# Kernel tuning notes

Measured on AMD Instinct MI355X. Metric: run time of the kernel, lower is better.

## Reference

```python
import jax, jax.numpy as jnp
import numpy as np

B, H, W = 4, 64, 64
DIM, NH, HD = 768, 12, 64
MLP_DIM = 3072
WS = 14
EPS = 1e-6
SCALE = HD ** -0.5
QMIN, QMAX = -128.0, 127.0  # 8-bit signed fake-quant range


def fake_quant(x, s):
    # uniform quant-dequant with straight-through estimator
    q = jnp.clip(jnp.round(x / s), QMIN, QMAX) * s
    return x + jax.lax.stop_gradient(q - x)


def layer_norm(x, w, b):
    mu = jnp.mean(x, axis=-1, keepdims=True)
    var = jnp.var(x, axis=-1, keepdims=True)
    return (x - mu) * jax.lax.rsqrt(var + EPS) * w + b


def qlinear(x, w, b, a_s, w_s):
    # PreQuantizedLayer: fake-quant input activation and weight, then linear
    return fake_quant(x, a_s) @ fake_quant(w, w_s).T + b


def _attention(xw, qkv_w, qkv_b, proj_w, proj_b, rel_pos_h, rel_pos_w, a_s, w_s):
    Bw = xw.shape[0]
    N = WS * WS
    qkv = qlinear(xw.reshape(Bw, N, DIM), qkv_w, qkv_b, a_s[4], w_s[0])
    qkv = qkv.reshape(Bw, N, 3, NH, HD).transpose(2, 0, 3, 1, 4).reshape(3, Bw * NH, N, HD)
    q = fake_quant(qkv[0], a_s[0])
    k = fake_quant(qkv[1], a_s[1])
    v = fake_quant(qkv[2], a_s[2])
    attn = jnp.einsum('bqc,bkc->bqk', q * SCALE, k)  # (Bw*NH, N, N)
    # decomposed relative position bias (q_size == k_size == WS)
    idx = jnp.arange(WS)[:, None] - jnp.arange(WS)[None, :] + (WS - 1)
    Rh = rel_pos_h[idx]  # (WS, WS, HD)
    Rw = rel_pos_w[idx]
    r_q = q.reshape(Bw * NH, WS, WS, HD)
    rel_h = jnp.einsum('bhwc,hkc->bhwk', r_q, Rh)
    rel_w = jnp.einsum('bhwc,wkc->bhwk', r_q, Rw)
    attn = (attn.reshape(-1, WS, WS, WS, WS) + rel_h[..., :, None] + rel_w[..., None, :]).reshape(-1, N, N)
    attn = fake_quant(jax.nn.softmax(attn, axis=-1), a_s[3])
    out = jnp.einsum('bqk,bkc->bqc', attn, v)
    out = out.reshape(Bw, NH, WS, WS, HD).transpose(0, 2, 3, 1, 4).reshape(Bw, WS, WS, DIM)
    return qlinear(out, proj_w, proj_b, a_s[5], w_s[1])


def _forward(x, ln1_w, ln1_b, ln2_w, ln2_b, qkv_w, qkv_b, proj_w, proj_b,
             lin1_w, lin1_b, lin2_w, lin2_b, rel_pos_h, rel_pos_w, act_scales, w_scales):
    shortcut = x
    h = layer_norm(x, ln1_w, ln1_b)
    pad_h = (WS - H % WS) % WS
    pad_w = (WS - W % WS) % WS
    Hp, Wp = H + pad_h, W + pad_w
    hp = jnp.pad(h, ((0, 0), (0, pad_h), (0, pad_w), (0, 0)))
    win = hp.reshape(B, Hp // WS, WS, Wp // WS, WS, DIM).transpose(0, 1, 3, 2, 4, 5).reshape(-1, WS, WS, DIM)
    win = _attention(win, qkv_w, qkv_b, proj_w, proj_b, rel_pos_h, rel_pos_w, act_scales, w_scales)
    hp = win.reshape(B, Hp // WS, Wp // WS, WS, WS, DIM).transpose(0, 1, 3, 2, 4, 5).reshape(B, Hp, Wp, DIM)
    x = shortcut + hp[:, :H, :W, :]
    y = layer_norm(x, ln2_w, ln2_b)
    y = qlinear(y, lin1_w, lin1_b, act_scales[6], w_scales[2])
    y = jax.nn.gelu(y, approximate=False)
    y = qlinear(y, lin2_w, lin2_b, act_scales[7], w_scales[3])
    return x + y


def setup_inputs() -> dict:
    key = jax.random.key(0)
    ks = jax.random.split(key, 12)
    def w(k, shape, std=0.02):
        return jax.random.normal(k, shape, dtype=jnp.float32) * std
    return {
        'x': jax.random.normal(ks[0], (B, H, W, DIM), dtype=jnp.float32),
        'ln1_w': jnp.ones((DIM,), jnp.float32), 'ln1_b': jnp.zeros((DIM,), jnp.float32),
        'ln2_w': jnp.ones((DIM,), jnp.float32), 'ln2_b': jnp.zeros((DIM,), jnp.float32),
        'qkv_w': w(ks[1], (3 * DIM, DIM)), 'qkv_b': jnp.zeros((3 * DIM,), jnp.float32),
        'proj_w': w(ks[2], (DIM, DIM)), 'proj_b': jnp.zeros((DIM,), jnp.float32),
        'lin1_w': w(ks[3], (MLP_DIM, DIM)), 'lin1_b': jnp.zeros((MLP_DIM,), jnp.float32),
        'lin2_w': w(ks[4], (DIM, MLP_DIM)), 'lin2_b': jnp.zeros((DIM,), jnp.float32),
        'rel_pos_h': w(ks[5], (2 * WS - 1, HD)), 'rel_pos_w': w(ks[6], (2 * WS - 1, HD)),
        'act_scales': jax.random.uniform(ks[7], (8,), jnp.float32, 0.01, 0.06),
        'w_scales': jax.random.uniform(ks[8], (4,), jnp.float32, 0.0005, 0.003),
    }


def reference(x, ln1_w, ln1_b, ln2_w, ln2_b, qkv_w, qkv_b, proj_w, proj_b,
              lin1_w, lin1_b, lin2_w, lin2_b, rel_pos_h, rel_pos_w, act_scales, w_scales):
    return _forward(x, ln1_w, ln1_b, ln2_w, ln2_b, qkv_w, qkv_b, proj_w, proj_b,
                    lin1_w, lin1_b, lin2_w, lin2_b, rel_pos_h, rel_pos_w, act_scales, w_scales)
```

## Files before the change

### kernel.cpp

```cpp
#include <hip/hip_runtime.h>
#include <cstdint>


typedef int   v4i __attribute__((ext_vector_type(4)));
typedef float v4f __attribute__((ext_vector_type(4)));
typedef short v8s __attribute__((ext_vector_type(8)));
typedef int8_t i8;

__device__ __forceinline__ i8 satq(float x) {
  float q = rintf(x);
  q = fminf(127.f, fmaxf(-128.f, q));
  return (i8)(int)q;
}

__device__ __forceinline__ void gload16(const i8* g, i8* l) {
  __builtin_amdgcn_global_load_lds((const __attribute__((address_space(1))) void*)g,
                                   (__attribute__((address_space(3))) void*)l, 16, 0, 0);
}

__device__ __forceinline__ int pack4(const i8* q) {
  return ((int)(unsigned char)q[0]) | ((int)(unsigned char)q[1] << 8) |
         ((int)(unsigned char)q[2] << 16) | ((int)(unsigned char)q[3] << 24);
}

__device__ __forceinline__ float fast_gelu(float v) {
  float x = fabsf(v) * 0.70710678118654752f;
  float t = __builtin_amdgcn_rcpf(fmaf(0.3275911f, x, 1.0f));
  float s = fmaf(1.061405429f, t, -1.453152027f);
  s = fmaf(s, t, 1.421413741f);
  s = fmaf(s, t, -0.284496736f);
  s = fmaf(s, t, 0.254829592f);
  s = s * t;
  float e = __expf(-x * x);
  float erfa = fmaf(-s, e, 1.0f);
  float erfs = copysignf(erfa, v);
  float hv = 0.5f * v;
  return fmaf(hv, erfs, hv);
}

__global__ __launch_bounds__(256) void k_wquant(const float* __restrict__ w,
                                                i8* __restrict__ o, int n16,
                                                const float* __restrict__ wsc, int sidx) {
  int i = blockIdx.x * 256 + threadIdx.x;
  if (i >= n16) return;
  float inv = 1.0f / wsc[sidx];
  const float4* src = (const float4*)w + (size_t)i * 4;
  i8 buf[16];
#pragma unroll
  for (int t = 0; t < 4; t++) {
    float4 f = src[t];
    buf[t*4+0] = satq(f.x * inv); buf[t*4+1] = satq(f.y * inv);
    buf[t*4+2] = satq(f.z * inv); buf[t*4+3] = satq(f.w * inv);
  }
  *(v4i*)(o + (size_t)i * 16) = *(v4i*)buf;
}

__global__ __launch_bounds__(256) void k_relpack(const float* __restrict__ rph,
    const float* __restrict__ rpw, short* __restrict__ TB) {
  int g = blockIdx.x * 256 + threadIdx.x;
  if (g >= 1024) return;
  int lane = g & 63, c = g >> 6;
  int p = c & 1, ks = (c >> 1) & 1, nt = (c >> 2) & 1, tb = c >> 3;
  const float* src = tb ? rpw : rph;
  int n = nt * 16 + (lane & 15);
  int k0 = ks * 32 + (lane >> 4) * 8;
  short outv[8];
#pragma unroll
  for (int j = 0; j < 8; j++) {
    float v = (n < 27) ? src[n * 64 + k0 + j] : 0.f;
    unsigned u = __float_as_uint(v);
    unsigned hi = (u + 0x7fffu + ((u >> 16) & 1u)) >> 16;
    if (p == 0) outv[j] = (short)hi;
    else {
      float lof = v - __uint_as_float(hi << 16);
      unsigned ul = __float_as_uint(lof);
      outv[j] = (short)((ul + 0x7fffu + ((ul >> 16) & 1u)) >> 16);
    }
  }
  *(v8s*)(TB + (size_t)c * 512 + lane * 8) = *(v8s*)outv;
}

__global__ __launch_bounds__(256) void k_ln1(const float* __restrict__ x,
    const float* __restrict__ w, const float* __restrict__ b,
    const float* __restrict__ as, i8* __restrict__ outq) {
  int wt = blockIdx.x * 4 + (threadIdx.x >> 6);
  int lane = threadIdx.x & 63;
  int win = wt / 196, tok = wt - win * 196;
  int bb = win / 25, wrem = win - bb * 25, wh = wrem / 5, ww = wrem - wh * 5;
  int r = tok / 14, c = tok - r * 14;
  int y = wh * 14 + r, xx = ww * 14 + c;
  i8* dst = outq + (size_t)wt * 768 + lane * 12;
  if (y >= 64 || xx >= 64) {
    ((int*)dst)[0] = 0; ((int*)dst)[1] = 0; ((int*)dst)[2] = 0;
    return;
  }
  const float* row = x + (((size_t)bb * 64 + y) * 64 + xx) * 768 + lane * 12;
  float v[12];
  *(float4*)(v)     = *(const float4*)(row);
  *(float4*)(v + 4) = *(const float4*)(row + 4);
  *(float4*)(v + 8) = *(const float4*)(row + 8);
  float s = 0.f, ss = 0.f;
#pragma unroll
  for (int j = 0; j < 12; j++) { s += v[j]; ss += v[j] * v[j]; }
#pragma unroll
  for (int off = 1; off < 64; off <<= 1) { s += __shfl_xor(s, off); ss += __shfl_xor(ss, off); }
  float mu = s * (1.0f / 768.0f);
  float var = ss * (1.0f / 768.0f) - mu * mu;
  float rstd = 1.0f / sqrtf(var + 1e-6f);
  float inv = 1.0f / as[4];
  float wv[12], bv[12];
  *(float4*)(wv)     = *(const float4*)(w + lane * 12);
  *(float4*)(wv + 4) = *(const float4*)(w + lane * 12 + 4);
  *(float4*)(wv + 8) = *(const float4*)(w + lane * 12 + 8);
  *(float4*)(bv)     = *(const float4*)(b + lane * 12);
  *(float4*)(bv + 4) = *(const float4*)(b + lane * 12 + 4);
  *(float4*)(bv + 8) = *(const float4*)(b + lane * 12 + 8);
  i8 q[12];
#pragma unroll
  for (int j = 0; j < 12; j++) q[j] = satq(((v[j] - mu) * rstd * wv[j] + bv[j]) * inv);
  ((int*)dst)[0] = pack4(q); ((int*)dst)[1] = pack4(q + 4); ((int*)dst)[2] = pack4(q + 8);
}

__global__ __launch_bounds__(256) void k_ln2(const float* __restrict__ x2,
    const float* __restrict__ w, const float* __restrict__ b,
    const float* __restrict__ as, i8* __restrict__ outq) {
  int tokg = blockIdx.x * 4 + (threadIdx.x >> 6);
  int lane = threadIdx.x & 63;
  const float* row = x2 + (size_t)tokg * 768 + lane * 12;
  float v[12];
  *(float4*)(v)     = *(const float4*)(row);
  *(float4*)(v + 4) = *(const float4*)(row + 4);
  *(float4*)(v + 8) = *(const float4*)(row + 8);
  float s = 0.f, ss = 0.f;
#pragma unroll
  for (int j = 0; j < 12; j++) { s += v[j]; ss += v[j] * v[j]; }
#pragma unroll
  for (int off = 1; off < 64; off <<= 1) { s += __shfl_xor(s, off); ss += __shfl_xor(ss, off); }
  float mu = s * (1.0f / 768.0f);
  float var = ss * (1.0f / 768.0f) - mu * mu;
  float rstd = 1.0f / sqrtf(var + 1e-6f);
  float inv = 1.0f / as[6];
  float wv[12], bv[12];
  *(float4*)(wv)     = *(const float4*)(w + lane * 12);
  *(float4*)(wv + 4) = *(const float4*)(w + lane * 12 + 4);
  *(float4*)(wv + 8) = *(const float4*)(w + lane * 12 + 8);
  *(float4*)(bv)     = *(const float4*)(b + lane * 12);
  *(float4*)(bv + 4) = *(const float4*)(b + lane * 12 + 4);
  *(float4*)(bv + 8) = *(const float4*)(b + lane * 12 + 8);
  i8* dst = outq + (size_t)tokg * 768 + lane * 12;
  i8 q[12];
#pragma unroll
  for (int j = 0; j < 12; j++) q[j] = satq(((v[j] - mu) * rstd * wv[j] + bv[j]) * inv);
  ((int*)dst)[0] = pack4(q); ((int*)dst)[1] = pack4(q + 4); ((int*)dst)[2] = pack4(q + 8);
}

template <class Epi>
__global__ __launch_bounds__(256) void k_gemm(const i8* __restrict__ A, const i8* __restrict__ B,
                                              int M, int N, int K, Epi epi) {
  __shared__ __align__(16) i8 As[2][128 * 64];
  __shared__ __align__(16) i8 Bs[2][128 * 64];
  const int tid = threadIdx.x;
  const int lane = tid & 63, wave = tid >> 6;
  const int quad = lane >> 4, lc = lane & 15;
  const int wr = wave >> 1, wc = wave & 1;
  const long bm = (long)blockIdx.y * 128, bn = (long)blockIdx.x * 128;
  const v4i vz = {0, 0, 0, 0};
  v4i acc[4][4];
#pragma unroll
  for (int i = 0; i < 4; i++)
#pragma unroll
    for (int j = 0; j < 4; j++) acc[i][j] = vz;

  const int r0 = tid >> 2, c0 = tid & 3;
  long rA0 = bm + r0;      if (rA0 >= M) rA0 = 0;
  long rA1 = bm + r0 + 64; if (rA1 >= M) rA1 = 0;
  const i8* pA0 = A + rA0 * (size_t)K + c0 * 16;
  const i8* pA1 = A + rA1 * (size_t)K + c0 * 16;
  const i8* pB0 = B + (bn + r0)      * (size_t)K + c0 * 16;
  const i8* pB1 = B + (bn + r0 + 64) * (size_t)K + c0 * 16;

  auto stage = [&](int buf) {
    gload16(pA0, As[buf] + tid * 16); gload16(pA1, As[buf] + 4096 + tid * 16);
    gload16(pB0, Bs[buf] + tid * 16); gload16(pB1, Bs[buf] + 4096 + tid * 16);
    pA0 += 64; pA1 += 64; pB0 += 64; pB1 += 64;
  };

  stage(0);
  __syncthreads();
  const int nt = K >> 6;
  int cur = 0;
  for (int t = 0; t < nt; ++t) {
    if (t + 1 < nt) stage(cur ^ 1);
    v4i af[4], bf[4];
#pragma unroll
    for (int i = 0; i < 4; i++) af[i] = *(const v4i*)(As[cur] + (wr * 64 + i * 16 + lc) * 64 + quad * 16);
#pragma unroll
    for (int j = 0; j < 4; j++) bf[j] = *(const v4i*)(Bs[cur] + (wc * 64 + j * 16 + lc) * 64 + quad * 16);
#pragma unroll
    for (int i = 0; i < 4; i++)
#pragma unroll
      for (int j = 0; j < 4; j++)
        acc[i][j] = __builtin_amdgcn_mfma_i32_16x16x64_i8(af[i], bf[j], acc[i][j], 0, 0, 0);
    if (t + 1 < nt) __syncthreads();
    cur ^= 1;
  }
  Epi e = epi;
  e.init();
#pragma unroll
  for (int i = 0; i < 4; i++) {
    int gm0 = (int)bm + wr * 64 + i * 16 + quad * 4;
#pragma unroll
    for (int j = 0; j < 4; j++) {
      int gn = (int)bn + wc * 64 + j * 16 + lc;
      if (gm0 < M) e.store4(acc[i][j], gm0, gn);
    }
  }
}

struct EpiQKV {
  const float* as; const float* wsc; const float* bias;
  i8 *qq, *kq, *vt;
  float sab, invq, invk, invv;
  __device__ void init() {
    sab = as[4] * wsc[0]; invq = 1.f / as[0]; invk = 1.f / as[1]; invv = 1.f / as[2];
  }
  __device__ void store4(const v4i a, int m0, int n) {
    int t = n / 768, rem = n - t * 768;
    int head = rem >> 6, ch = rem & 63;
    int win = m0 / 196, tok0 = m0 - win * 196;
    size_t bh = (size_t)win * 12 + head;
    float bv = bias[n];
    if (t == 2) {
      i8 q[4];
#pragma unroll
      for (int r = 0; r < 4; r++) q[r] = satq(((float)a[r] * sab + bv) * invv);
      *(int*)(vt + (bh * 64 + ch) * 256 + tok0) = pack4(q);
    } else {
      float inv = (t == 0) ? invq : invk;
      i8* dst = (t == 0 ? qq : kq) + (bh * 196 + tok0) * 64 + ch;
#pragma unroll
      for (int r = 0; r < 4; r++) dst[(size_t)r * 64] = satq(((float)a[r] * sab + bv) * inv);
    }
  }
};

struct EpiProj {
  const float* as; const float* wsc; const float* bias; const float* x0; float* out;
  float sab;
  __device__ void init() { sab = as[5] * wsc[1]; }
  __device__ void store4(const v4i a, int m0, int n) {
    int win = m0 / 196, tok0 = m0 - win * 196;
    int bb = win / 25, wrem = win - bb * 25, wh = wrem / 5, ww = wrem - wh * 5;
    float bv = bias[n];
#pragma unroll
    for (int r = 0; r < 4; r++) {
      int tok = tok0 + r;
      int rr = tok / 14, cc = tok - rr * 14;
      int y = wh * 14 + rr, xx = ww * 14 + cc;
      if (y < 64 && xx < 64) {
        size_t o = (((size_t)bb * 64 + y) * 64 + xx) * 768 + n;
        out[o] = (float)a[r] * sab + bv + x0[o];
      }
    }
  }
};

struct EpiLin1 {
  const float* as; const float* wsc; const float* bias; i8* outq;
  float sab, invg;
  __device__ void init() { sab = as[6] * wsc[2]; invg = 1.f / as[7]; }
  __device__ void store4(const v4i a, int m0, int n) {
    float bv = bias[n];
#pragma unroll
    for (int r = 0; r < 4; r++) {
      float v = fmaf((float)a[r], sab, bv);
      outq[(size_t)(m0 + r) * 3072 + n] = satq(fast_gelu(v) * invg);
    }
  }
};

struct EpiLin2 {
  const float* as; const float* wsc; const float* bias; float* out;
  float sab;
  __device__ void init() { sab = as[7] * wsc[3]; }
  __device__ void store4(const v4i a, int m0, int n) {
    float bv = bias[n];
#pragma unroll
    for (int r = 0; r < 4; r++) {
      size_t o = (size_t)(m0 + r) * 768 + n;
      out[o] += (float)a[r] * sab + bv;
    }
  }
};

__global__ __launch_bounds__(64, 4) void k_attn(const i8* __restrict__ qq, const i8* __restrict__ kq,
    const i8* __restrict__ vt, const short* __restrict__ TB,
    const float* __restrict__ as, i8* __restrict__ outq) {
  __shared__ __align__(16) i8 Ps[16 * 272];
  __shared__ float relS[16][66];
  const int t = blockIdx.x, bh = blockIdx.y;
  const int win = bh / 12, head = bh - win * 12;
  const int lane = threadIdx.x;
  const int quad = lane >> 4, lc = lane & 15;
  const float s0 = as[0];
  const float ssc = s0 * as[1] * 0.125f;
  const float invs3 = 1.0f / as[3];
  const float oscale = as[2] * as[3] / as[5];

  for (int idx = lane; idx < 256; idx += 64)
    *(int*)(Ps + (idx >> 4) * 272 + 192 + (idx & 15) * 4) = 0;

  unsigned ckhp[4] = {0, 0, 0, 0}, ckwp[4] = {0, 0, 0, 0};
#pragma unroll
  for (int f = 0; f < 13; f++) {
    int col = f * 16 + lc; if (col > 195) col = 195;
    int kh = col / 14, kw = col - kh * 14;
    ckhp[f >> 2] |= (unsigned)kh << ((f & 3) * 8);
    ckwp[f >> 2] |= (unsigned)kw << ((f & 3) * 8);
  }

  const v8s* TBv = (const v8s*)TB;
  const v4i vz = {0, 0, 0, 0};

  {
    int arow = t * 16 + lc; if (arow > 195) arow = 195;
    const i8* qrow = qq + ((size_t)bh * 196 + arow) * 64;
    v8s af[2];
#pragma unroll
    for (int ks = 0; ks < 2; ks++) {
      const i8* p = qrow + ks * 32 + quad * 8;
#pragma unroll
      for (int j = 0; j < 8; j++)
        af[ks][j] = (short)(__float_as_uint((float)p[j]) >> 16);
    }
    v4f rh0 = {0,0,0,0}, rh1 = {0,0,0,0}, rw0 = {0,0,0,0}, rw1 = {0,0,0,0};
#pragma unroll
    for (int ks = 0; ks < 2; ks++)
#pragma unroll
      for (int p2 = 0; p2 < 2; p2++) {
        rh0 = __builtin_amdgcn_mfma_f32_16x16x32_bf16(af[ks], TBv[(0*4 + ks*2 + p2)*64 + lane], rh0, 0, 0, 0);
        rh1 = __builtin_amdgcn_mfma_f32_16x16x32_bf16(af[ks], TBv[(1*4 + ks*2 + p2)*64 + lane], rh1, 0, 0, 0);
        rw0 = __builtin_amdgcn_mfma_f32_16x16x32_bf16(af[ks], TBv[(2*4 + ks*2 + p2)*64 + lane], rw0, 0, 0, 0);
        rw1 = __builtin_amdgcn_mfma_f32_16x16x32_bf16(af[ks], TBv[(3*4 + ks*2 + p2)*64 + lane], rw1, 0, 0, 0);
      }
#pragma unroll
    for (int r = 0; r < 4; r++) {
      int rl = quad * 4 + r;
      relS[rl][lc]      = rh0[r] * s0;
      relS[rl][16 + lc] = rh1[r] * s0;
      relS[rl][32 + lc] = rw0[r] * s0;
      relS[rl][48 + lc] = rw1[r] * s0;
    }
  }

  v4i aq = *(const v4i*)(qq + ((size_t)bh * 196 + t * 16 + lc) * 64 + quad * 16);
  v4i sacc[13];
#pragma unroll
  for (int f = 0; f < 13; f++) {
    v4i bk = *(const v4i*)(kq + ((size_t)bh * 196 + f * 16 + lc) * 64 + quad * 16);
    sacc[f] = __builtin_amdgcn_mfma_i32_16x16x64_i8(aq, bk, vz, 0, 0, 0);
  }

#pragma unroll
  for (int r = 0; r < 4; r++) {
    int rl = quad * 4 + r;
    int row = t * 16 + rl;
    int qh = row / 14, qw = row - qh * 14;
    const float* rH = &relS[rl][13 + qh];
    const float* rW = &relS[rl][32 + 13 + qw];
    float L[13];
#pragma unroll
    for (int f = 0; f < 13; f++) {
      int kh = (int)((ckhp[f >> 2] >> ((f & 3) * 8)) & 0xffu);
      int kw = (int)((ckwp[f >> 2] >> ((f & 3) * 8)) & 0xffu);
      L[f] = ((f < 12) | (lc < 4)) ? fmaf((float)sacc[f][r], ssc, rH[-kh] + rW[-kw]) : -1e30f;
    }
    float mx = L[0];
#pragma unroll
    for (int f = 1; f < 13; f++) mx = fmaxf(mx, L[f]);
#pragma unroll
    for (int off = 1; off < 16; off <<= 1) mx = fmaxf(mx, __shfl_xor(mx, off));
    float sum = 0.f;
#pragma unroll
    for (int f = 0; f < 13; f++) { float e = __expf(L[f] - mx); L[f] = e; sum += e; }
#pragma unroll
    for (int off = 1; off < 16; off <<= 1) sum += __shfl_xor(sum, off);
    float cq = (1.0f / sum) * invs3;
#pragma unroll
    for (int f = 0; f < 13; f++)
      Ps[rl * 272 + f * 16 + lc] = satq(L[f] * cq);
  }

  v4i oacc[4];
#pragma unroll
  for (int nt = 0; nt < 4; nt++) oacc[nt] = vz;
#pragma unroll
  for (int kc = 0; kc < 4; kc++) {
    v4i ap = *(const v4i*)(Ps + lc * 272 + kc * 64 + quad * 16);
#pragma unroll
    for (int nt = 0; nt < 4; nt++) {
      v4i bv = *(const v4i*)(vt + ((size_t)bh * 64 + nt * 16 + lc) * 256 + kc * 64 + quad * 16);
      oacc[nt] = __builtin_amdgcn_mfma_i32_16x16x64_i8(ap, bv, oacc[nt], 0, 0, 0);
    }
  }
#pragma unroll
  for (int nt = 0; nt < 4; nt++) {
    int ch = nt * 16 + lc;
#pragma unroll
    for (int r = 0; r < 4; r++) {
      int row = t * 16 + quad * 4 + r;
      if (row < 196)
        outq[((size_t)win * 196 + row) * 768 + head * 64 + ch] = satq((float)oacc[nt][r] * oscale);
    }
  }
}

extern "C" void kernel_launch(void* const* d_in, const int* in_sizes, int n_in,
                              void* d_out, int out_size, void* d_ws, size_t ws_size,
                              hipStream_t stream) {
  const float* x     = (const float*)d_in[0];
  const float* ln1w  = (const float*)d_in[1];
  const float* ln1b  = (const float*)d_in[2];
  const float* ln2w  = (const float*)d_in[3];
  const float* ln2b  = (const float*)d_in[4];
  const float* qkvw  = (const float*)d_in[5];
  const float* qkvb  = (const float*)d_in[6];
  const float* projw = (const float*)d_in[7];
  const float* projb = (const float*)d_in[8];
  const float* lin1w = (const float*)d_in[9];
  const float* lin1b = (const float*)d_in[10];
  const float* lin2w = (const float*)d_in[11];
  const float* lin2b = (const float*)d_in[12];
  const float* rph   = (const float*)d_in[13];
  const float* rpw   = (const float*)d_in[14];
  const float* as    = (const float*)d_in[15];
  const float* wsc   = (const float*)d_in[16];
  float* out = (float*)d_out;

  char* ws = (char*)d_ws;
  i8* big    = (i8*)ws;
  i8* qq     = big;
  i8* kq     = big + 15052800;
  i8* vt     = big + 30105600;
  short* TB  = (short*)(big + 49766400);
  i8* mlpq   = big;
  i8* creg   = (i8*)(ws + 50331648);
  i8* winq   = creg;
  i8* attno  = creg;
  i8* yq     = creg;
  i8* wqb    = (i8*)(ws + 65384448);
  i8* qkvwq  = wqb;
  i8* projwq = wqb + 1769472;
  i8* lin1wq = projwq + 589824;
  i8* lin2wq = lin1wq + 2359296;

  k_wquant<<<(110592 + 255) / 256, 256, 0, stream>>>(qkvw,  qkvwq,  110592, wsc, 0);
  k_wquant<<<( 36864 + 255) / 256, 256, 0, stream>>>(projw, projwq,  36864, wsc, 1);
  k_wquant<<<(147456 + 255) / 256, 256, 0, stream>>>(lin1w, lin1wq, 147456, wsc, 2);
  k_wquant<<<(147456 + 255) / 256, 256, 0, stream>>>(lin2w, lin2wq, 147456, wsc, 3);
  k_relpack<<<4, 256, 0, stream>>>(rph, rpw, TB);

  k_ln1<<<4900, 256, 0, stream>>>(x, ln1w, ln1b, as, winq);

  { EpiQKV e{as, wsc, qkvb, qq, kq, vt};
    k_gemm<EpiQKV><<<dim3(18, 154), 256, 0, stream>>>(winq, qkvwq, 19600, 2304, 768, e); }

  k_attn<<<dim3(13, 1200), 64, 0, stream>>>(qq, kq, vt, TB, as, attno);

  { EpiProj e{as, wsc, projb, x, out};
    k_gemm<EpiProj><<<dim3(6, 154), 256, 0, stream>>>(attno, projwq, 19600, 768, 768, e); }

  k_ln2<<<4096, 256, 0, stream>>>(out, ln2w, ln2b, as, yq);

  { EpiLin1 e{as, wsc, lin1b, mlpq};
    k_gemm<EpiLin1><<<dim3(24, 128), 256, 0, stream>>>(yq, lin1wq, 16384, 3072, 768, e); }

  { EpiLin2 e{as, wsc, lin2b, out};
    k_gemm<EpiLin2><<<dim3(6, 128), 256, 0, stream>>>(mlpq, lin2wq, 16384, 768, 3072, e); }
}
```

Baseline: 493.1 us.

## Triple-buffer GEMM LDS with XOR swizzle and vectorized transposed epilogues

The int8 GEMM moves from a double-buffered to a triple-buffered LDS pipeline, using explicit vmcnt waits and one barrier per K-step so loads stay further ahead of the MFMAs. The LDS layout gets an XOR swizzle on the 16-byte column chunks to cut bank conflicts on fragment reads. The MFMA operands are swapped so each lane holds 4 consecutive output columns, which lets the epilogues use float4 and packed int32 stores instead of scattered scalar ones. The cost is 50% more LDS per block, which may lower occupancy, and the V-transpose store in the QKV epilogue becomes byte-scattered.

```diff
diff --git a/kernel.cpp b/kernel.cpp
--- a/kernel.cpp
+++ b/kernel.cpp
@@ -157,8 +157,8 @@
 template <class Epi>
 __global__ __launch_bounds__(256) void k_gemm(const i8* __restrict__ A, const i8* __restrict__ B,
                                               int M, int N, int K, Epi epi) {
-  __shared__ __align__(16) i8 As[2][128 * 64];
-  __shared__ __align__(16) i8 Bs[2][128 * 64];
+  __shared__ __align__(16) i8 As[3][8192];
+  __shared__ __align__(16) i8 Bs[3][8192];
   const int tid = threadIdx.x;
   const int lane = tid & 63, wave = tid >> 6;
   const int quad = lane >> 4, lc = lane & 15;
@@ -172,12 +172,13 @@
     for (int j = 0; j < 4; j++) acc[i][j] = vz;
 
   const int r0 = tid >> 2, c0 = tid & 3;
+  const int cs = c0 ^ ((r0 >> 1) & 3);
   long rA0 = bm + r0;      if (rA0 >= M) rA0 = 0;
   long rA1 = bm + r0 + 64; if (rA1 >= M) rA1 = 0;
-  const i8* pA0 = A + rA0 * (size_t)K + c0 * 16;
-  const i8* pA1 = A + rA1 * (size_t)K + c0 * 16;
-  const i8* pB0 = B + (bn + r0)      * (size_t)K + c0 * 16;
-  const i8* pB1 = B + (bn + r0 + 64) * (size_t)K + c0 * 16;
+  const i8* pA0 = A + rA0 * (size_t)K + cs * 16;
+  const i8* pA1 = A + rA1 * (size_t)K + cs * 16;
+  const i8* pB0 = B + (bn + r0)      * (size_t)K + cs * 16;
+  const i8* pB1 = B + (bn + r0 + 64) * (size_t)K + cs * 16;
 
   auto stage = [&](int buf) {
     gload16(pA0, As[buf] + tid * 16); gload16(pA1, As[buf] + 4096 + tid * 16);
@@ -185,34 +186,45 @@
     pA0 += 64; pA1 += 64; pB0 += 64; pB1 += 64;
   };
 
-  stage(0);
-  __syncthreads();
+  const int xq16 = (quad ^ ((lc >> 1) & 3)) * 16;
+
+  auto compute = [&](int buf) {
+    v4i af[4], bf[4];
+#pragma unroll
+    for (int i = 0; i < 4; i++) af[i] = *(const v4i*)(As[buf] + (wr * 64 + i * 16 + lc) * 64 + xq16);
+#pragma unroll
+    for (int j = 0; j < 4; j++) bf[j] = *(const v4i*)(Bs[buf] + (wc * 64 + j * 16 + lc) * 64 + xq16);
+#pragma unroll
+    for (int i = 0; i < 4; i++)
+#pragma unroll
+      for (int j = 0; j < 4; j++)
+        acc[i][j] = __builtin_amdgcn_mfma_i32_16x16x64_i8(bf[j], af[i], acc[i][j], 0, 0, 0);
+  };
+
   const int nt = K >> 6;
-  int cur = 0;
-  for (int t = 0; t < nt; ++t) {
-    if (t + 1 < nt) stage(cur ^ 1);
-    v4i af[4], bf[4];
-#pragma unroll
-    for (int i = 0; i < 4; i++) af[i] = *(const v4i*)(As[cur] + (wr * 64 + i * 16 + lc) * 64 + quad * 16);
-#pragma unroll
-    for (int j = 0; j < 4; j++) bf[j] = *(const v4i*)(Bs[cur] + (wc * 64 + j * 16 + lc) * 64 + quad * 16);
-#pragma unroll
-    for (int i = 0; i < 4; i++)
-#pragma unroll
-      for (int j = 0; j < 4; j++)
-        acc[i][j] = __builtin_amdgcn_mfma_i32_16x16x64_i8(af[i], bf[j], acc[i][j], 0, 0, 0);
-    if (t + 1 < nt) __syncthreads();
-    cur ^= 1;
-  }
+  stage(0); stage(1);
+  int cb = 0, sb = 2;
+  for (int t = 0; t < nt - 1; ++t) {
+    asm volatile("s_waitcnt vmcnt(4)" ::: "memory");
+    __builtin_amdgcn_s_barrier();
+    asm volatile("" ::: "memory");
+    if (t + 2 < nt) { stage(sb); if (++sb == 3) sb = 0; }
+    compute(cb); if (++cb == 3) cb = 0;
+  }
+  asm volatile("s_waitcnt vmcnt(0)" ::: "memory");
+  __builtin_amdgcn_s_barrier();
+  asm volatile("" ::: "memory");
+  compute(cb);
+
   Epi e = epi;
   e.init();
 #pragma unroll
   for (int i = 0; i < 4; i++) {
-    int gm0 = (int)bm + wr * 64 + i * 16 + quad * 4;
+    int gm = (int)bm + wr * 64 + i * 16 + lc;
 #pragma unroll
     for (int j = 0; j < 4; j++) {
-      int gn = (int)bn + wc * 64 + j * 16 + lc;
-      if (gm0 < M) e.store4(acc[i][j], gm0, gn);
+      int gn0 = (int)bn + wc * 64 + j * 16 + quad * 4;
+      if (gm < M) e.store4(acc[i][j], gm, gn0);
     }
   }
 }
@@ -224,22 +236,23 @@
   __device__ void init() {
     sab = as[4] * wsc[0]; invq = 1.f / as[0]; invk = 1.f / as[1]; invv = 1.f / as[2];
   }
-  __device__ void store4(const v4i a, int m0, int n) {
-    int t = n / 768, rem = n - t * 768;
-    int head = rem >> 6, ch = rem & 63;
-    int win = m0 / 196, tok0 = m0 - win * 196;
+  __device__ void store4(const v4i a, int m, int n0) {
+    int t = n0 / 768, rem = n0 - t * 768;
+    int head = rem >> 6, ch0 = rem & 63;
+    int win = m / 196, tok = m - win * 196;
     size_t bh = (size_t)win * 12 + head;
-    float bv = bias[n];
+    float4 bv = *(const float4*)(bias + n0);
+    const float* bp = (const float*)&bv;
     if (t == 2) {
-      i8 q[4];
-#pragma unroll
-      for (int r = 0; r < 4; r++) q[r] = satq(((float)a[r] * sab + bv) * invv);
-      *(int*)(vt + (bh * 64 + ch) * 256 + tok0) = pack4(q);
+#pragma unroll
+      for (int r = 0; r < 4; r++)
+        vt[(bh * 64 + ch0 + r) * 256 + tok] = satq(((float)a[r] * sab + bp[r]) * invv);
     } else {
       float inv = (t == 0) ? invq : invk;
-      i8* dst = (t == 0 ? qq : kq) + (bh * 196 + tok0) * 64 + ch;
-#pragma unroll
-      for (int r = 0; r < 4; r++) dst[(size_t)r * 64] = satq(((float)a[r] * sab + bv) * inv);
+      i8 q[4];
+#pragma unroll
+      for (int r = 0; r < 4; r++) q[r] = satq(((float)a[r] * sab + bp[r]) * inv);
+      *(int*)((t == 0 ? qq : kq) + (bh * 196 + tok) * 64 + ch0) = pack4(q);
     }
   }
 };
@@ -248,20 +261,21 @@
   const float* as; const float* wsc; const float* bias; const float* x0; float* out;
   float sab;
   __device__ void init() { sab = as[5] * wsc[1]; }
-  __device__ void store4(const v4i a, int m0, int n) {
-    int win = m0 / 196, tok0 = m0 - win * 196;
+  __device__ void store4(const v4i a, int m, int n0) {
+    int win = m / 196, tok = m - win * 196;
     int bb = win / 25, wrem = win - bb * 25, wh = wrem / 5, ww = wrem - wh * 5;
-    float bv = bias[n];
-#pragma unroll
-    for (int r = 0; r < 4; r++) {
-      int tok = tok0 + r;
-      int rr = tok / 14, cc = tok - rr * 14;
-      int y = wh * 14 + rr, xx = ww * 14 + cc;
-      if (y < 64 && xx < 64) {
-        size_t o = (((size_t)bb * 64 + y) * 64 + xx) * 768 + n;
-        out[o] = (float)a[r] * sab + bv + x0[o];
-      }
-    }
+    int rr = tok / 14, cc = tok - rr * 14;
+    int y = wh * 14 + rr, xx = ww * 14 + cc;
+    if (y >= 64 || xx >= 64) return;
+    size_t o = (((size_t)bb * 64 + y) * 64 + xx) * 768 + n0;
+    float4 bv = *(const float4*)(bias + n0);
+    float4 xv = *(const float4*)(x0 + o);
+    float4 ov;
+    ov.x = (float)a[0] * sab + bv.x + xv.x;
+    ov.y = (float)a[1] * sab + bv.y + xv.y;
+    ov.z = (float)a[2] * sab + bv.z + xv.z;
+    ov.w = (float)a[3] * sab + bv.w + xv.w;
+    *(float4*)(out + o) = ov;
   }
 };
 
@@ -269,13 +283,16 @@
   const float* as; const float* wsc; const float* bias; i8* outq;
   float sab, invg;
   __device__ void init() { sab = as[6] * wsc[2]; invg = 1.f / as[7]; }
-  __device__ void store4(const v4i a, int m0, int n) {
-    float bv = bias[n];
+  __device__ void store4(const v4i a, int m, int n0) {
+    float4 bv = *(const float4*)(bias + n0);
+    const float* bp = (const float*)&bv;
+    i8 q[4];
 #pragma unroll
     for (int r = 0; r < 4; r++) {
-      float v = fmaf((float)a[r], sab, bv);
-      outq[(size_t)(m0 + r) * 3072 + n] = satq(fast_gelu(v) * invg);
-    }
+      float v = fmaf((float)a[r], sab, bp[r]);
+      q[r] = satq(fast_gelu(v) * invg);
+    }
+    *(int*)(outq + (size_t)m * 3072 + n0) = pack4(q);
   }
 };
 
@@ -283,13 +300,15 @@
   const float* as; const float* wsc; const float* bias; float* out;
   float sab;
   __device__ void init() { sab = as[7] * wsc[3]; }
-  __device__ void store4(const v4i a, int m0, int n) {
-    float bv = bias[n];
-#pragma unroll
-    for (int r = 0; r < 4; r++) {
-      size_t o = (size_t)(m0 + r) * 768 + n;
-      out[o] += (float)a[r] * sab + bv;
-    }
+  __device__ void store4(const v4i a, int m, int n0) {
+    size_t o = (size_t)m * 768 + n0;
+    float4 bv = *(const float4*)(bias + n0);
+    float4 ov = *(const float4*)(out + o);
+    ov.x += (float)a[0] * sab + bv.x;
+    ov.y += (float)a[1] * sab + bv.y;
+    ov.z += (float)a[2] * sab + bv.z;
+    ov.w += (float)a[3] * sab + bv.w;
+    *(float4*)(out + o) = ov;
   }
 };
 
```

Result: faster. 477.8 us (-3.1%).
